# Optimization experiments

Measured on AMD Instinct MI355X. Metric: run time of the kernel, lower is better.

The kernel has to match this reference:

```python
import jax, jax.numpy as jnp
import numpy as np
from jax import lax

SCORE_THRESH = 0.05
NMS_THRESH = 0.5
DETECTIONS_PER_IMG = 100
MIN_SIZE = 0.01
AREA_THRESH = 0.0
BOX_W = (10.0, 10.0, 5.0, 5.0)
BBOX_XFORM_CLIP = float(np.log(1000.0 / 16.0))


def setup_inputs() -> dict:
    key = jax.random.key(0)
    B, N, C = 8, 4000, 91
    H, W = 800, 1333
    k1, k2, k3 = jax.random.split(key, 3)
    # scale logits so a realistic fraction of softmax scores exceed score_thresh
    class_logits = jax.random.normal(k1, (B * N, C), jnp.float32) * 2.0
    box_regression = jax.random.normal(k2, (B * N, C * 4), jnp.float32)
    u = jax.random.uniform(k3, (B, N, 4), jnp.float32)
    x1 = u[..., 0] * (W - 50)
    y1 = u[..., 1] * (H - 50)
    bw = u[..., 2] * 200.0 + 4.0
    bh = u[..., 3] * 200.0 + 4.0
    proposals = jnp.stack([x1, y1, jnp.minimum(x1 + bw, W), jnp.minimum(y1 + bh, H)], axis=-1)
    return {"class_logits": class_logits, "box_regression": box_regression,
            "proposals": proposals, "image_h": H, "image_w": W}


def _decode(rel, props):
    # torchvision BoxCoder.decode: props [P,4], rel [P, C*4] -> [P, C, 4]
    w = props[:, 2] - props[:, 0]
    h = props[:, 3] - props[:, 1]
    cx = props[:, 0] + 0.5 * w
    cy = props[:, 1] + 0.5 * h
    rel = rel.reshape(rel.shape[0], -1, 4)
    dx = rel[..., 0] / BOX_W[0]
    dy = rel[..., 1] / BOX_W[1]
    dw = jnp.minimum(rel[..., 2] / BOX_W[2], BBOX_XFORM_CLIP)
    dh = jnp.minimum(rel[..., 3] / BOX_W[3], BBOX_XFORM_CLIP)
    pcx = dx * w[:, None] + cx[:, None]
    pcy = dy * h[:, None] + cy[:, None]
    pw = jnp.exp(dw) * w[:, None]
    ph = jnp.exp(dh) * h[:, None]
    return jnp.stack([pcx - 0.5 * pw, pcy - 0.5 * ph, pcx + 0.5 * pw, pcy + 0.5 * ph], axis=-1)


def _nms_image(boxes, scores, labels_f, valid, off_unit):
    # greedy batched NMS (class-offset trick) producing first DETECTIONS_PER_IMG survivors
    NEG = -1e9
    s0 = jnp.where(valid, scores, NEG)
    ob = boxes + (labels_f * off_unit)[:, None]  # per-class coordinate offset
    areas = (ob[:, 2] - ob[:, 0]) * (ob[:, 3] - ob[:, 1])

    def step(s, _):
        i = jnp.argmax(s)
        sc = s[i]
        ok = sc > (NEG / 2)
        obi = ob[i]
        ix1 = jnp.maximum(obi[0], ob[:, 0])
        iy1 = jnp.maximum(obi[1], ob[:, 1])
        ix2 = jnp.minimum(obi[2], ob[:, 2])
        iy2 = jnp.minimum(obi[3], ob[:, 3])
        inter = jnp.maximum(ix2 - ix1, 0.0) * jnp.maximum(iy2 - iy1, 0.0)
        ai = (obi[2] - obi[0]) * (obi[3] - obi[1])
        iou = inter / jnp.maximum(ai + areas - inter, 1e-9)
        sup = (iou > NMS_THRESH) & ok
        s = jnp.where(sup, NEG, s).at[i].set(NEG)
        return s, (i, jnp.where(ok, sc, 0.0), ok)

    _, (idx, out_sc, ok) = lax.scan(step, s0, None, length=DETECTIONS_PER_IMG)
    out_boxes = boxes[idx] * ok[:, None]
    out_labels = jnp.where(ok, labels_f[idx], 0.0)
    areas_out = (out_boxes[:, 2] - out_boxes[:, 0]) * (out_boxes[:, 3] - out_boxes[:, 1])
    keep = ok & (areas_out >= AREA_THRESH)
    return out_boxes * keep[:, None], out_sc * keep, jnp.where(keep, out_labels, 0.0), keep


def reference(class_logits, box_regression, proposals, image_h, image_w):
    B, N, _ = proposals.shape
    C = class_logits.shape[-1]
    pred_boxes = _decode(box_regression, proposals.reshape(B * N, 4)).reshape(B, N, C, 4)
    pred_scores = jax.nn.softmax(class_logits, axis=-1).reshape(B, N, C)
    # clip boxes to image
    x = jnp.clip(pred_boxes[..., 0::2], 0.0, float(image_w))
    y = jnp.clip(pred_boxes[..., 1::2], 0.0, float(image_h))
    pred_boxes = jnp.stack([x[..., 0], y[..., 0], x[..., 1], y[..., 1]], axis=-1)
    # drop background class 0, flatten (proposal, class) pairs
    M = N * (C - 1)
    boxes = pred_boxes[:, :, 1:, :].reshape(B, M, 4)
    scores = pred_scores[:, :, 1:].reshape(B, M)
    labels_f = jnp.broadcast_to(jnp.arange(1, C, dtype=boxes.dtype)[None, :], (N, C - 1)).reshape(M)
    ws = boxes[..., 2] - boxes[..., 0]
    hs = boxes[..., 3] - boxes[..., 1]
    valid = (scores > SCORE_THRESH) & (ws >= MIN_SIZE) & (hs >= MIN_SIZE)
    off_unit = float(max(image_h, image_w)) + 1.0
    out_boxes, out_scores, out_labels_f, keep = jax.vmap(
        lambda b, s, v: _nms_image(b, s, labels_f, v, off_unit))(boxes, scores, valid)
    return out_boxes, out_scores, out_labels_f.astype(jnp.int32), keep
```

## Files before the change

kernel.cpp:

```cpp
#include <hip/hip_runtime.h>
#include <stdint.h>

typedef uint32_t u32;
typedef unsigned long long u64;

#define NB 8
#define NPER 4000
#define NC 91
#define NCLS 90
#define NDET 100
#define CHUNKS 64
#define RPB 63
#define LBIN 16
#define CCAP 63
#define BINCAP 512
#define SURVCAP 9216
#define NSFIX (NCLS * NDET)
#define FKCAP 1024
#define VPT 36
#define NBIN 1152
#define SLO 0x3D4CCCCEu
#define SSH 15

__device__ __forceinline__ float4 decode_clip(float4 rel, float w, float h,
                                              float cx, float cy, float W, float H) {
  const float XCLIP = 4.135166556742356f;
  float dx = rel.x / 10.0f;
  float dy = rel.y / 10.0f;
  float dw = fminf(rel.z / 5.0f, XCLIP);
  float dh = fminf(rel.w / 5.0f, XCLIP);
  float qcx = dx * w + cx;
  float qcy = dy * h + cy;
  float qw = expf(dw) * w;
  float qh = expf(dh) * h;
  float x1 = qcx - 0.5f * qw, y1 = qcy - 0.5f * qh;
  float x2 = qcx + 0.5f * qw, y2 = qcy + 0.5f * qh;
  x1 = fminf(fmaxf(x1, 0.0f), W);
  x2 = fminf(fmaxf(x2, 0.0f), W);
  y1 = fminf(fmaxf(y1, 0.0f), H);
  y2 = fminf(fmaxf(y2, 0.0f), H);
  return make_float4(x1, y1, x2, y2);
}

__device__ __forceinline__ u64 rdlane64(u64 v, int sl) {
  u32 lo = (u32)__builtin_amdgcn_readlane((int)(u32)v, sl);
  u32 hi = (u32)__builtin_amdgcn_readlane((int)(u32)(v >> 32), sl);
  return ((u64)hi << 32) | (u64)lo;
}

__device__ __forceinline__ void emit_row(int r, int rl, int lane, float sA, float sB,
    float W, float H, const float4* __restrict__ props4, const float4* __restrict__ breg4,
    u32* s_cnt, u64 (*s_key)[LBIN], float4 (*s_box)[LBIN],
    size_t chbase, u64* __restrict__ bins_key, float4* __restrict__ bins_box) {
  bool eA_ok = (lane >= 1) && (sA > 0.05f);
  bool eB_ok = (lane < NC - 64) && (sB > 0.05f);
  if (!(eA_ok || eB_ok)) return;
  float4 p = props4[r];
  float w = p.z - p.x, h = p.w - p.y;
  float cx = p.x + 0.5f * w, cy = p.y + 0.5f * h;
  if (eA_ok) {
    float4 raw = decode_clip(breg4[(size_t)r * NC + lane], w, h, cx, cy, W, H);
    if (((raw.z - raw.x) >= 0.01f) && ((raw.w - raw.y) >= 0.01f)) {
      int ci = lane - 1;
      u32 orig = (u32)(rl * NCLS + ci);
      u64 key = ((u64)__float_as_uint(sA) << 22) | (u64)(0x3FFFFFu - orig);
      u32 lp = atomicAdd(&s_cnt[ci], 1u);
      if (lp < LBIN) { s_key[ci][lp] = key; s_box[ci][lp] = raw; }
      else if (lp < CCAP) {
        size_t o = (chbase + ci) * CCAP + lp;
        bins_key[o] = key; bins_box[o] = raw;
      }
    }
  }
  if (eB_ok) {
    float4 raw = decode_clip(breg4[(size_t)r * NC + 64 + lane], w, h, cx, cy, W, H);
    if (((raw.z - raw.x) >= 0.01f) && ((raw.w - raw.y) >= 0.01f)) {
      int ci = 63 + lane;
      u32 orig = (u32)(rl * NCLS + ci);
      u64 key = ((u64)__float_as_uint(sB) << 22) | (u64)(0x3FFFFFu - orig);
      u32 lp = atomicAdd(&s_cnt[ci], 1u);
      if (lp < LBIN) { s_key[ci][lp] = key; s_box[ci][lp] = raw; }
      else if (lp < CCAP) {
        size_t o = (chbase + ci) * CCAP + lp;
        bins_key[o] = key; bins_box[o] = raw;
      }
    }
  }
}

__global__ __launch_bounds__(1024) void k_score(const float* __restrict__ logits,
    const float* __restrict__ boxreg, const float* __restrict__ props,
    const int* __restrict__ dh, const int* __restrict__ dw,
    u32* cnt_g, u64* bins_key, float4* bins_box) {
  __shared__ u64 s_key[NCLS][LBIN];
  __shared__ float4 s_box[NCLS][LBIN];
  __shared__ u32 s_cnt[NCLS];
  int tid = threadIdx.x;
  int b = blockIdx.x / CHUNKS;
  int chunk = blockIdx.x % CHUNKS;
  int wave = tid >> 6, lane = tid & 63;
  if (tid < NCLS) s_cnt[tid] = 0u;
  __syncthreads();

  float H = (float)dh[0], W = (float)dw[0];
  const float4* props4 = (const float4*)props;
  const float4* breg4 = (const float4*)boxreg;
  size_t chbase = ((size_t)(b * CHUNKS + chunk)) * NCLS;

  for (int rloc = wave; rloc < RPB; rloc += 32) {
    int rloc1 = rloc + 16;
    int rl0 = chunk * RPB + rloc;
    int rl1 = chunk * RPB + rloc1;
    bool v0 = (rl0 < NPER);
    bool v1 = (rloc1 < RPB) && (rl1 < NPER);
    int r0 = b * NPER + (v0 ? rl0 : 0);
    int r1 = b * NPER + (v1 ? rl1 : 0);
    const float* l0 = logits + (size_t)r0 * NC;
    const float* l1 = logits + (size_t)r1 * NC;
    float xA0 = l0[lane];
    float xA1 = l1[lane];
    float xB0 = (lane < NC - 64) ? l0[64 + lane] : -3.0e38f;
    float xB1 = (lane < NC - 64) ? l1[64 + lane] : -3.0e38f;
    float mx0 = fmaxf(xA0, xB0);
    float mx1 = fmaxf(xA1, xB1);
    for (int o = 32; o; o >>= 1) {
      mx0 = fmaxf(mx0, __shfl_xor(mx0, o));
      mx1 = fmaxf(mx1, __shfl_xor(mx1, o));
    }
    float eA0 = expf(xA0 - mx0);
    float eA1 = expf(xA1 - mx1);
    float eB0 = (lane < NC - 64) ? expf(xB0 - mx0) : 0.0f;
    float eB1 = (lane < NC - 64) ? expf(xB1 - mx1) : 0.0f;
    float sm0 = eA0 + eB0;
    float sm1 = eA1 + eB1;
    for (int o = 32; o; o >>= 1) {
      sm0 += __shfl_xor(sm0, o);
      sm1 += __shfl_xor(sm1, o);
    }
    if (v0) emit_row(r0, rl0, lane, eA0 / sm0, eB0 / sm0, W, H, props4, breg4,
                     s_cnt, s_key, s_box, chbase, bins_key, bins_box);
    if (v1) emit_row(r1, rl1, lane, eA1 / sm1, eB1 / sm1, W, H, props4, breg4,
                     s_cnt, s_key, s_box, chbase, bins_key, bins_box);
  }
  __syncthreads();
  if (tid < NCLS) cnt_g[chbase + tid] = s_cnt[tid];
  for (int idx = tid; idx < NCLS * LBIN; idx += 1024) {
    int ci = idx / LBIN, j = idx % LBIN;
    if ((u32)j < s_cnt[ci]) {
      size_t o = (chbase + ci) * CCAP + (u32)j;
      bins_key[o] = s_key[ci][j];
      bins_box[o] = s_box[ci][j];
    }
  }
}

__global__ __launch_bounds__(256) void k_nms_class(const u32* __restrict__ cnt_g,
    const u64* __restrict__ bins_key, const float4* __restrict__ bins_box,
    u64* skey, float4* sbox, const int* __restrict__ dh, const int* __restrict__ dw) {
  __shared__ u64 k[BINCAP];
  __shared__ float4 boxu[BINCAP];
  __shared__ u64 ks[BINCAP];
  __shared__ float4 boxs[BINCAP];
  __shared__ float4 s_sb[NDET];
  __shared__ float s_sa[NDET];
  __shared__ u64 s_sk[NDET];
  __shared__ u32 s_sid[NDET];
  __shared__ u32 s_off[64];
  __shared__ u32 s_c[64];
  __shared__ u32 s_n;

  int b = blockIdx.x / NCLS;
  int ci = blockIdx.x % NCLS;
  int tid = threadIdx.x;
  u64* outk = skey + (size_t)b * SURVCAP + (size_t)ci * NDET;
  float4* outb = sbox + (size_t)b * SURVCAP + (size_t)ci * NDET;

  if (tid < 64) {
    u32 c = cnt_g[((size_t)(b * CHUNKS + tid)) * NCLS + ci];
    if (c > CCAP) c = CCAP;
    s_c[tid] = c;
    u32 inc = c;
    for (int o = 1; o < 64; o <<= 1) {
      u32 v = __shfl_up(inc, o);
      if (tid >= o) inc += v;
    }
    s_off[tid] = inc - c;
    if (tid == 63) s_n = (inc > BINCAP) ? BINCAP : inc;
  }
  __syncthreads();
  int n = (int)s_n;
  if (n <= 0) {
    for (int i = tid; i < NDET; i += 256) outk[i] = 0ull;
    return;
  }
  {
    int chunk = tid & 63, start = tid >> 6;
    u32 cc = s_c[chunk], of = s_off[chunk];
    size_t src = (((size_t)(b * CHUNKS + chunk)) * NCLS + ci) * CCAP;
    for (u32 i = (u32)start; i < cc; i += 4) {
      u32 d = of + i;
      if (d < (u32)BINCAP) { k[d] = bins_key[src + i]; boxu[d] = bins_box[src + i]; }
    }
  }
  __syncthreads();
  for (int i = tid; i < n; i += 256) {
    u64 ki = k[i];
    u32 rank = 0;
    int j = 0;
    for (; j + 4 <= n; j += 4) {
      rank += (k[j] > ki) ? 1u : 0u;
      rank += (k[j + 1] > ki) ? 1u : 0u;
      rank += (k[j + 2] > ki) ? 1u : 0u;
      rank += (k[j + 3] > ki) ? 1u : 0u;
    }
    for (; j < n; ++j) rank += (k[j] > ki) ? 1u : 0u;
    ks[rank] = ki;
    boxs[rank] = boxu[i];
  }
  __syncthreads();
  if (tid >= 64) return;

  float H = (float)dh[0], W = (float)dw[0];
  float loff = (fmaxf(H, W) + 1.0f) * (float)(ci + 1);
  int lane = tid;
  int S = 0;
  for (int base = 0; base < n && S < NDET; base += 64) {
    int i = base + lane;
    bool have = (i < n);
    u64 mykey = 0ull;
    float4 Bb = make_float4(0.f, 0.f, 0.f, 0.f);
    float aB = 0.f;
    if (have) {
      mykey = ks[i];
      float4 raw = boxs[i];
      Bb = make_float4(raw.x + loff, raw.y + loff, raw.z + loff, raw.w + loff);
      aB = (Bb.z - Bb.x) * (Bb.w - Bb.y);
    }
    u64 myword = 0ull;
    int lim = n - base; if (lim > 64) lim = 64;
#pragma unroll 4
    for (int m = 0; m < lim; ++m) {
      float4 As = boxs[base + m];
      float ax = As.x + loff, ay = As.y + loff;
      float az = As.z + loff, aw = As.w + loff;
      float aA = (az - ax) * (aw - ay);
      float ix1 = fmaxf(ax, Bb.x), iy1 = fmaxf(ay, Bb.y);
      float ix2 = fminf(az, Bb.z), iy2 = fminf(aw, Bb.w);
      float inter = fmaxf(ix2 - ix1, 0.0f) * fmaxf(iy2 - iy1, 0.0f);
      float iou = inter / fmaxf(aA + aB - inter, 1e-9f);
      if (iou > 0.5f) myword |= (1ull << m);
    }
    bool alive = have;
    for (int s = 0; s < S; ++s) {
      float4 A = s_sb[s];
      float aA = s_sa[s];
      float ix1 = fmaxf(A.x, Bb.x), iy1 = fmaxf(A.y, Bb.y);
      float ix2 = fminf(A.z, Bb.z), iy2 = fminf(A.w, Bb.w);
      float inter = fmaxf(ix2 - ix1, 0.0f) * fmaxf(iy2 - iy1, 0.0f);
      float iou = inter / fmaxf(aA + aB - inter, 1e-9f);
      if (alive && iou > 0.5f) alive = false;
    }
    u64 mask = __ballot(alive);
    u64 sel = 0ull;
    while (mask != 0ull && S + (int)__popcll(sel) < NDET) {
      int j0 = __builtin_amdgcn_readfirstlane(__builtin_ctzll(mask));
      sel |= (1ull << j0);
      u64 row = rdlane64(myword, j0);
      mask &= ~row;
    }
    if ((sel >> lane) & 1ull) {
      int rank = S + (int)__popcll(sel & ((1ull << lane) - 1ull));
      s_sb[rank] = Bb; s_sa[rank] = aB; s_sk[rank] = mykey; s_sid[rank] = (u32)i;
    }
    S += (int)__popcll(sel);
  }
  for (int i2 = lane; i2 < NDET; i2 += 64) {
    if (i2 < S) {
      outk[i2] = s_sk[i2];
      outb[i2] = boxs[s_sid[i2]];
    } else {
      outk[i2] = 0ull;
    }
  }
}

__global__ __launch_bounds__(256) void k_top(const u64* __restrict__ skey,
    const float4* __restrict__ sbox, float* out) {
  __shared__ u32 hist[NBIN];
  __shared__ u64 fk[FKCAP];
  __shared__ u32 fs[FKCAP];
  __shared__ u64 okey[NDET];
  __shared__ u32 osrc[NDET];
  __shared__ u32 s_cnt[2];
  __shared__ u32 s_bin;

  int b = blockIdx.x;
  int tid = threadIdx.x;
  const u64* kb = skey + (size_t)b * SURVCAP;

  u32 sc[VPT];
#pragma unroll
  for (int v = 0; v < VPT; ++v) {
    u32 j = (u32)tid + (u32)v * 256u;
    sc[v] = (j < NSFIX) ? (u32)(kb[j] >> 22) : 0u;
  }
  for (int i = tid; i < NBIN; i += 256) hist[i] = 0u;
  if (tid == 0) { s_cnt[0] = 0; s_cnt[1] = 0; }
  __syncthreads();

#pragma unroll
  for (int v = 0; v < VPT; ++v) {
    u32 s = sc[v];
    if (s > SLO) atomicAdd(&hist[(s - SLO) >> SSH], 1u);
  }
  __syncthreads();

  if (tid < 64) {
    int lane = tid;
    int base = lane * (NBIN / 64);
    u32 csum = 0;
#pragma unroll
    for (int kk2 = 0; kk2 < NBIN / 64; ++kk2) csum += hist[base + kk2];
    u32 suf = csum;
    for (int o = 1; o < 64; o <<= 1) {
      u32 v = __shfl_down(suf, o);
      if (lane + o < 64) suf += v;
    }
    u64 m = __ballot(suf >= NDET);
    int B = 0;
    if (m) {
      int c = 63 - __builtin_clzll(m);
      u32 rest = (c < 63) ? (u32)__shfl((int)suf, c + 1) : 0u;
      u32 acc = rest;
      int cb = c * (NBIN / 64);
      for (int kk2 = (NBIN / 64) - 1; kk2 >= 0; --kk2) {
        acc += hist[cb + kk2];
        if (acc >= NDET) { B = cb + kk2; break; }
      }
    }
    if (lane == 0) s_bin = (u32)B;
  }
  __syncthreads();
  u32 B = s_bin;

#pragma unroll
  for (int v = 0; v < VPT; ++v) {
    u32 s = sc[v];
    if (s > SLO && ((s - SLO) >> SSH) > B) {
      u32 j = (u32)tid + (u32)v * 256u;
      u32 p = atomicAdd(&s_cnt[0], 1u);
      if (p < FKCAP) { fk[p] = kb[j]; fs[p] = j; }
    }
  }
  __syncthreads();
  if (tid == 0) s_cnt[1] = s_cnt[0];
  __syncthreads();
#pragma unroll
  for (int v = 0; v < VPT; ++v) {
    u32 s = sc[v];
    if (s > SLO && ((s - SLO) >> SSH) == B) {
      u32 j = (u32)tid + (u32)v * 256u;
      u32 p = atomicAdd(&s_cnt[1], 1u);
      if (p < FKCAP) { fk[p] = kb[j]; fs[p] = j; }
    }
  }
  __syncthreads();
  u32 tot = s_cnt[1];
  if (tot > FKCAP) tot = FKCAP;
  if (tid >= 64) return;

  for (int i = tid; i < NDET; i += 64) okey[i] = 0ull;
  for (int i = tid; i < (int)tot; i += 64) {
    u64 ki = fk[i];
    u32 rank = 0;
    for (int j = 0; j < (int)tot; ++j) rank += (fk[j] > ki) ? 1u : 0u;
    if (rank < NDET) { okey[rank] = ki; osrc[rank] = fs[i]; }
  }
  for (int i = tid; i < NDET; i += 64) {
    u64 key = okey[i];
    float b0 = 0.f, b1 = 0.f, b2 = 0.f, b3 = 0.f, sc2 = 0.f, lb = 0.f, kp = 0.f;
    if (key) {
      float4 bx = sbox[(size_t)b * SURVCAP + osrc[i]];
      b0 = bx.x; b1 = bx.y; b2 = bx.z; b3 = bx.w;
      sc2 = __uint_as_float((u32)(key >> 22));
      u32 orig = 0x3FFFFFu - (u32)(key & 0x3FFFFFu);
      lb = (float)(orig % NCLS + 1u);
      kp = 1.0f;
    }
    float* ob = out + ((size_t)b * NDET + i) * 4;
    ob[0] = b0; ob[1] = b1; ob[2] = b2; ob[3] = b3;
    out[NB * NDET * 4 + b * NDET + i] = sc2;
    out[NB * NDET * 5 + b * NDET + i] = lb;
    out[NB * NDET * 6 + b * NDET + i] = kp;
  }
}

extern "C" void kernel_launch(void* const* d_in, const int* in_sizes, int n_in,
                              void* d_out, int out_size, void* d_ws, size_t ws_size,
                              hipStream_t stream) {
  const float* logits = (const float*)d_in[0];
  const float* boxreg = (const float*)d_in[1];
  const float* props  = (const float*)d_in[2];
  const int* dh = (const int*)d_in[3];
  const int* dw = (const int*)d_in[4];
  float* out = (float*)d_out;

  char* ws = (char*)d_ws;
  u32* cnt_g = (u32*)ws;
  char* p0 = ws + (((size_t)NB * CHUNKS * NCLS * 4 + 255) & ~(size_t)255);
  u64* bins_key = (u64*)p0;
  char* p1 = p0 + (size_t)NB * CHUNKS * NCLS * CCAP * 8;
  float4* bins_box = (float4*)p1;
  char* p2 = p1 + (size_t)NB * CHUNKS * NCLS * CCAP * 16;
  u64* skey = (u64*)p2;
  float4* sbox = (float4*)(p2 + (size_t)NB * SURVCAP * 8);
  (void)ws_size;

  k_score<<<NB * CHUNKS, 1024, 0, stream>>>(logits, boxreg, props, dh, dw,
                                            cnt_g, bins_key, bins_box);
  k_nms_class<<<NB * NCLS, 256, 0, stream>>>(cnt_g, bins_key, bins_box,
                                             skey, sbox, dh, dw);
  k_top<<<NB, 256, 0, stream>>>(skey, sbox, out);
}
```

Before: 156.9 us.

## Replace per-chunk shared-memory bins with global per-class atomic pools

The scoring kernel now appends candidates straight into a per-image, per-class global pool using global atomic counters, rather than staging them in shared-memory bins per chunk and then flushing. The NMS kernel reads one contiguous pool per class instead of prefix-summing 64 chunk counts and gathering scattered bins. This removes the shared staging, the flush pass and the gather logic, but adds contended global atomics, a memset launch, and slot order that is no longer deterministic (sorting by key restores the order).

```diff
diff --git a/kernel.cpp b/kernel.cpp
--- a/kernel.cpp
+++ b/kernel.cpp
@@ -11,8 +11,7 @@
 #define NDET 100
 #define CHUNKS 64
 #define RPB 63
-#define LBIN 16
-#define CCAP 63
+#define PCAP 512
 #define BINCAP 512
 #define SURVCAP 9216
 #define NSFIX (NCLS * NDET)
@@ -50,8 +49,7 @@
 
 __device__ __forceinline__ void emit_row(int r, int rl, int lane, float sA, float sB,
     float W, float H, const float4* __restrict__ props4, const float4* __restrict__ breg4,
-    u32* s_cnt, u64 (*s_key)[LBIN], float4 (*s_box)[LBIN],
-    size_t chbase, u64* __restrict__ bins_key, float4* __restrict__ bins_box) {
+    u32* __restrict__ pc, u64* __restrict__ pk, float4* __restrict__ pb) {
   bool eA_ok = (lane >= 1) && (sA > 0.05f);
   bool eB_ok = (lane < NC - 64) && (sB > 0.05f);
   if (!(eA_ok || eB_ok)) return;
@@ -64,11 +62,10 @@
       int ci = lane - 1;
       u32 orig = (u32)(rl * NCLS + ci);
       u64 key = ((u64)__float_as_uint(sA) << 22) | (u64)(0x3FFFFFu - orig);
-      u32 lp = atomicAdd(&s_cnt[ci], 1u);
-      if (lp < LBIN) { s_key[ci][lp] = key; s_box[ci][lp] = raw; }
-      else if (lp < CCAP) {
-        size_t o = (chbase + ci) * CCAP + lp;
-        bins_key[o] = key; bins_box[o] = raw;
+      u32 slot = atomicAdd(&pc[ci], 1u);
+      if (slot < PCAP) {
+        size_t o = (size_t)ci * PCAP + slot;
+        pk[o] = key; pb[o] = raw;
       }
     }
   }
@@ -78,11 +75,10 @@
       int ci = 63 + lane;
       u32 orig = (u32)(rl * NCLS + ci);
       u64 key = ((u64)__float_as_uint(sB) << 22) | (u64)(0x3FFFFFu - orig);
-      u32 lp = atomicAdd(&s_cnt[ci], 1u);
-      if (lp < LBIN) { s_key[ci][lp] = key; s_box[ci][lp] = raw; }
-      else if (lp < CCAP) {
-        size_t o = (chbase + ci) * CCAP + lp;
-        bins_key[o] = key; bins_box[o] = raw;
+      u32 slot = atomicAdd(&pc[ci], 1u);
+      if (slot < PCAP) {
+        size_t o = (size_t)ci * PCAP + slot;
+        pk[o] = key; pb[o] = raw;
       }
     }
   }
@@ -91,21 +87,18 @@
 __global__ __launch_bounds__(1024) void k_score(const float* __restrict__ logits,
     const float* __restrict__ boxreg, const float* __restrict__ props,
     const int* __restrict__ dh, const int* __restrict__ dw,
-    u32* cnt_g, u64* bins_key, float4* bins_box) {
-  __shared__ u64 s_key[NCLS][LBIN];
-  __shared__ float4 s_box[NCLS][LBIN];
-  __shared__ u32 s_cnt[NCLS];
+    u32* pool_cnt, u64* pool_key, float4* pool_box) {
   int tid = threadIdx.x;
   int b = blockIdx.x / CHUNKS;
   int chunk = blockIdx.x % CHUNKS;
   int wave = tid >> 6, lane = tid & 63;
-  if (tid < NCLS) s_cnt[tid] = 0u;
-  __syncthreads();
 
   float H = (float)dh[0], W = (float)dw[0];
   const float4* props4 = (const float4*)props;
   const float4* breg4 = (const float4*)boxreg;
-  size_t chbase = ((size_t)(b * CHUNKS + chunk)) * NCLS;
+  u32* pc = pool_cnt + (size_t)b * NCLS;
+  u64* pk = pool_key + (size_t)b * NCLS * PCAP;
+  float4* pb = pool_box + (size_t)b * NCLS * PCAP;
 
   for (int rloc = wave; rloc < RPB; rloc += 32) {
     int rloc1 = rloc + 16;
@@ -138,24 +131,14 @@
       sm1 += __shfl_xor(sm1, o);
     }
     if (v0) emit_row(r0, rl0, lane, eA0 / sm0, eB0 / sm0, W, H, props4, breg4,
-                     s_cnt, s_key, s_box, chbase, bins_key, bins_box);
+                     pc, pk, pb);
     if (v1) emit_row(r1, rl1, lane, eA1 / sm1, eB1 / sm1, W, H, props4, breg4,
-                     s_cnt, s_key, s_box, chbase, bins_key, bins_box);
-  }
-  __syncthreads();
-  if (tid < NCLS) cnt_g[chbase + tid] = s_cnt[tid];
-  for (int idx = tid; idx < NCLS * LBIN; idx += 1024) {
-    int ci = idx / LBIN, j = idx % LBIN;
-    if ((u32)j < s_cnt[ci]) {
-      size_t o = (chbase + ci) * CCAP + (u32)j;
-      bins_key[o] = s_key[ci][j];
-      bins_box[o] = s_box[ci][j];
-    }
-  }
-}
-
-__global__ __launch_bounds__(256) void k_nms_class(const u32* __restrict__ cnt_g,
-    const u64* __restrict__ bins_key, const float4* __restrict__ bins_box,
+                     pc, pk, pb);
+  }
+}
+
+__global__ __launch_bounds__(256) void k_nms_class(const u32* __restrict__ pool_cnt,
+    const u64* __restrict__ pool_key, const float4* __restrict__ pool_box,
     u64* skey, float4* sbox, const int* __restrict__ dh, const int* __restrict__ dw) {
   __shared__ u64 k[BINCAP];
   __shared__ float4 boxu[BINCAP];
@@ -165,9 +148,6 @@
   __shared__ float s_sa[NDET];
   __shared__ u64 s_sk[NDET];
   __shared__ u32 s_sid[NDET];
-  __shared__ u32 s_off[64];
-  __shared__ u32 s_c[64];
-  __shared__ u32 s_n;
 
   int b = blockIdx.x / NCLS;
   int ci = blockIdx.x % NCLS;
@@ -175,32 +155,16 @@
   u64* outk = skey + (size_t)b * SURVCAP + (size_t)ci * NDET;
   float4* outb = sbox + (size_t)b * SURVCAP + (size_t)ci * NDET;
 
-  if (tid < 64) {
-    u32 c = cnt_g[((size_t)(b * CHUNKS + tid)) * NCLS + ci];
-    if (c > CCAP) c = CCAP;
-    s_c[tid] = c;
-    u32 inc = c;
-    for (int o = 1; o < 64; o <<= 1) {
-      u32 v = __shfl_up(inc, o);
-      if (tid >= o) inc += v;
-    }
-    s_off[tid] = inc - c;
-    if (tid == 63) s_n = (inc > BINCAP) ? BINCAP : inc;
-  }
-  __syncthreads();
-  int n = (int)s_n;
+  u32 cnt = pool_cnt[(size_t)b * NCLS + ci];
+  int n = (int)(cnt > PCAP ? PCAP : cnt);
   if (n <= 0) {
     for (int i = tid; i < NDET; i += 256) outk[i] = 0ull;
     return;
   }
-  {
-    int chunk = tid & 63, start = tid >> 6;
-    u32 cc = s_c[chunk], of = s_off[chunk];
-    size_t src = (((size_t)(b * CHUNKS + chunk)) * NCLS + ci) * CCAP;
-    for (u32 i = (u32)start; i < cc; i += 4) {
-      u32 d = of + i;
-      if (d < (u32)BINCAP) { k[d] = bins_key[src + i]; boxu[d] = bins_box[src + i]; }
-    }
+  size_t src = ((size_t)b * NCLS + ci) * PCAP;
+  for (int i = tid; i < n; i += 256) {
+    k[i] = pool_key[src + i];
+    boxu[i] = pool_box[src + i];
   }
   __syncthreads();
   for (int i = tid; i < n; i += 256) {
@@ -406,19 +370,21 @@
   float* out = (float*)d_out;
 
   char* ws = (char*)d_ws;
-  u32* cnt_g = (u32*)ws;
-  char* p0 = ws + (((size_t)NB * CHUNKS * NCLS * 4 + 255) & ~(size_t)255);
-  u64* bins_key = (u64*)p0;
-  char* p1 = p0 + (size_t)NB * CHUNKS * NCLS * CCAP * 8;
-  float4* bins_box = (float4*)p1;
-  char* p2 = p1 + (size_t)NB * CHUNKS * NCLS * CCAP * 16;
+  u32* pool_cnt = (u32*)ws;
+  char* p0 = ws + 4096;
+  u64* pool_key = (u64*)p0;
+  char* p1 = p0 + (size_t)NB * NCLS * PCAP * 8;
+  float4* pool_box = (float4*)p1;
+  char* p2 = p1 + (size_t)NB * NCLS * PCAP * 16;
   u64* skey = (u64*)p2;
   float4* sbox = (float4*)(p2 + (size_t)NB * SURVCAP * 8);
   (void)ws_size;
 
+  hipMemsetAsync(pool_cnt, 0, (size_t)NB * NCLS * sizeof(u32), stream);
+
   k_score<<<NB * CHUNKS, 1024, 0, stream>>>(logits, boxreg, props, dh, dw,
-                                            cnt_g, bins_key, bins_box);
-  k_nms_class<<<NB * NCLS, 256, 0, stream>>>(cnt_g, bins_key, bins_box,
+                                            pool_cnt, pool_key, pool_box);
+  k_nms_class<<<NB * NCLS, 256, 0, stream>>>(pool_cnt, pool_key, pool_box,
                                              skey, sbox, dh, dw);
   k_top<<<NB, 256, 0, stream>>>(skey, sbox, out);
 }
```

Measured after the change: 189.7 us. 1.21x slower.
